# Optimization experiments

Measured on AMD Instinct MI355X. Metric: run time of the kernel, lower is better.

## Reference

```python
import jax, jax.numpy as jnp
import numpy as np

B, C, H, W = 8, 256, 200, 200
D_IN, D_HID, D_OUT = 256, 1024, 40000

def setup_inputs() -> dict:
    key = jax.random.key(0)
    k1, k2, k3, k4, k5, k6 = jax.random.split(key, 6)
    x = jax.random.normal(k1, (B, C, H, W), dtype=jnp.float32)
    localization = jax.random.normal(k2, (B, D_IN), dtype=jnp.float32)
    # Linear params (PyTorch default init scale ~ 1/sqrt(fan_in))
    W1 = jax.random.normal(k3, (D_IN, D_HID), dtype=jnp.float32) / np.sqrt(D_IN)
    b1 = jax.random.normal(k4, (D_HID,), dtype=jnp.float32) / np.sqrt(D_IN)
    W2 = jax.random.normal(k5, (D_HID, D_OUT), dtype=jnp.float32) / np.sqrt(D_HID)
    b2 = jax.random.normal(k6, (D_OUT,), dtype=jnp.float32) / np.sqrt(D_HID)
    return {"x": x, "localization": localization, "W1": W1, "b1": b1, "W2": W2, "b2": b2}

def reference(x, localization, W1, b1, W2, b2):
    # MLP: Linear(256,1024) -> LeakyReLU(0.1) -> Linear(1024,40000)
    h = localization @ W1 + b1
    h = jnp.where(h >= 0, h, 0.1 * h)
    w = h @ W2 + b2                      # [B, 40000]
    w = w.reshape(x.shape[0], 200, 200)  # [B, 200, 200]
    # Vectorized form of the nested loop: x[i,j] += x[i,j] * w[i]
    return x * (1.0 + w[:, None, :, :])
```

## Files before the change

### kernel.cpp

```cpp
#include <hip/hip_runtime.h>

#define B_    8
#define D_IN  256
#define D_HID 1024
#define D_OUT 40000
#define HW4   10000
#define CHW4  2560000

typedef float f32x4 __attribute__((ext_vector_type(4)));

__global__ void mlp1_kernel(const float* __restrict__ loc,
                            const float* __restrict__ W1,
                            const float* __restrict__ b1,
                            float* __restrict__ hT) {
    __shared__ float red[256];
    int g    = blockIdx.x;
    int b    = g >> 4;
    int k0   = (g & 15) * 64;
    int w    = threadIdx.x >> 6;
    int lane = threadIdx.x & 63;
    int k    = k0 + lane;

    float acc = 0.0f;
    #pragma unroll 8
    for (int ii = 0; ii < 64; ++ii) {
        int i = w * 64 + ii;
        acc += loc[b * D_IN + i] * W1[i * D_HID + k];
    }
    red[threadIdx.x] = acc;
    __syncthreads();
    if (w == 0) {
        float s = red[lane] + red[64 + lane] + red[128 + lane] + red[192 + lane];
        s += b1[k];
        s = (s >= 0.0f) ? s : 0.1f * s;
        hT[k * B_ + b] = s;
    }
}

template<int KS>
__global__ void mlp2_partial_kernel(const float* __restrict__ hT,
                                    const float* __restrict__ W2,
                                    float* __restrict__ partial) {
    constexpr int CHUNK = D_HID / KS;
    int j4 = blockIdx.x * 64 + threadIdx.x;
    if (j4 >= HW4) return;
    int ks = blockIdx.y;
    int k0 = ks * CHUNK;
    const f32x4* __restrict__ W24 = (const f32x4*)W2;
    f32x4 acc[B_];
    #pragma unroll
    for (int b = 0; b < B_; ++b) acc[b] = (f32x4)0.0f;
    #pragma unroll 8
    for (int kk = 0; kk < CHUNK; ++kk) {
        int k = k0 + kk;
        f32x4 wv = __builtin_nontemporal_load(&W24[k * HW4 + j4]);
        const float* __restrict__ h = &hT[k * B_];
        #pragma unroll
        for (int b = 0; b < B_; ++b)
            acc[b] += wv * h[b];
    }
    f32x4* __restrict__ p4 = (f32x4*)partial;
    #pragma unroll
    for (int b = 0; b < B_; ++b)
        __builtin_nontemporal_store(acc[b], &p4[(ks * B_ + b) * HW4 + j4]);
}

template<int KS>
__global__ void mlp2_reduce_kernel(const float* __restrict__ partial,
                                   const float* __restrict__ b2,
                                   float* __restrict__ wmap) {
    int t = blockIdx.x * blockDim.x + threadIdx.x;
    if (t >= B_ * HW4) return;
    int b = t / HW4;
    int j4 = t - b * HW4;
    const f32x4* __restrict__ p4  = (const f32x4*)partial;
    const f32x4* __restrict__ b24 = (const f32x4*)b2;
    f32x4 s = b24[j4] + 1.0f;
    #pragma unroll
    for (int ks = 0; ks < KS; ++ks)
        s += __builtin_nontemporal_load(&p4[(ks * B_ + b) * HW4 + j4]);
    ((f32x4*)wmap)[b * HW4 + j4] = s;
}

__global__ void scale_kernel(const float* __restrict__ x,
                             const float* __restrict__ wmap,
                             float* __restrict__ out) {
    const int b = blockIdx.y;
    const int g = blockIdx.x * 256 + threadIdx.x;
    const unsigned p = (unsigned)g % HW4;

    const f32x4* __restrict__ x4 = (const f32x4*)x + (size_t)b * CHW4;
    f32x4* __restrict__ o4       = (f32x4*)out + (size_t)b * CHW4;
    const f32x4 wv = ((const f32x4*)wmap)[(size_t)b * HW4 + p];

    #pragma unroll 4
    for (int n = 0; n < 16; ++n) {
        int i = g + n * 160000;
        f32x4 xv = __builtin_nontemporal_load(&x4[i]);
        __builtin_nontemporal_store(xv * wv, &o4[i]);
    }
}

template<int KS>
static void launch_mlp2(const float* hT, const float* W2, const float* b2,
                        float* partial, float* wmap, hipStream_t stream) {
    dim3 g2(157, KS);
    mlp2_partial_kernel<KS><<<g2, 64, 0, stream>>>(hT, W2, partial);
    mlp2_reduce_kernel<KS><<<(B_ * HW4 + 255) / 256, 256, 0, stream>>>(partial, b2, wmap);
}

extern "C" void kernel_launch(void* const* d_in, const int* in_sizes, int n_in,
                              void* d_out, int out_size, void* d_ws, size_t ws_size,
                              hipStream_t stream) {
    const float* x   = (const float*)d_in[0];
    const float* loc = (const float*)d_in[1];
    const float* W1  = (const float*)d_in[2];
    const float* b1  = (const float*)d_in[3];
    const float* W2  = (const float*)d_in[4];
    const float* b2  = (const float*)d_in[5];
    float* out = (float*)d_out;

    float* hT      = (float*)d_ws;
    float* partial = (float*)((char*)d_ws + 32768);

    size_t base = 32768;
    int KS = 1;
    for (int cand = 8; cand >= 1; cand >>= 1) {
        size_t need = base + (size_t)(cand + 1) * B_ * D_OUT * sizeof(float);
        if (need <= ws_size) { KS = cand; break; }
    }
    float* wmap = (float*)((char*)d_ws + base
                           + (size_t)KS * B_ * D_OUT * sizeof(float));

    mlp1_kernel<<<128, 256, 0, stream>>>(loc, W1, b1, hT);

    switch (KS) {
        case 8:  launch_mlp2<8>(hT, W2, b2, partial, wmap, stream); break;
        case 4:  launch_mlp2<4>(hT, W2, b2, partial, wmap, stream); break;
        case 2:  launch_mlp2<2>(hT, W2, b2, partial, wmap, stream); break;
        default: launch_mlp2<1>(hT, W2, b2, partial, wmap, stream); break;
    }

    scale_kernel<<<dim3(625, 8), 256, 0, stream>>>(x, wmap, out);
}
```

Baseline: 162.5 us.

## Fuse MLP stages into one persistent kernel with atomic grid barriers

Merges the hidden-layer kernel, the W2 partial GEMV and the partial reduction into a single launch of one-wave blocks that coordinate through global atomic counters and spin-wait barriers. Ticketed blocks compute the hidden layer while the others wait on a completion counter. A grid-wide barrier separates the partial products from the reduction. This removes two kernel launches and their gaps, at the cost of spin-wait overhead, a memset, a fixed split count, and reliance on every block being co-resident.

New measurement: 410.2 us. +152.5%, slower.

```diff
diff --git a/kernel.cpp b/kernel.cpp
--- a/kernel.cpp
+++ b/kernel.cpp
@@ -6,80 +6,103 @@
 #define D_OUT 40000
 #define HW4   10000
 #define CHW4  2560000
+#define KS    8
+#define CHUNK 128
+#define NUNITS 1256
+#define RBLK  1250
 
 typedef float f32x4 __attribute__((ext_vector_type(4)));
+typedef unsigned long long u64;
 
-__global__ void mlp1_kernel(const float* __restrict__ loc,
+__device__ __forceinline__ void store16_agent(f32x4 v, f32x4* p) {
+    union { f32x4 v; u64 q[2]; } u; u.v = v;
+    u64* d = (u64*)p;
+    __hip_atomic_store(d,     u.q[0], __ATOMIC_RELAXED, __HIP_MEMORY_SCOPE_AGENT);
+    __hip_atomic_store(d + 1, u.q[1], __ATOMIC_RELAXED, __HIP_MEMORY_SCOPE_AGENT);
+}
+
+__global__ void mlpA_kernel(const float* __restrict__ loc,
                             const float* __restrict__ W1,
                             const float* __restrict__ b1,
-                            float* __restrict__ hT) {
-    __shared__ float red[256];
-    int g    = blockIdx.x;
-    int b    = g >> 4;
-    int k0   = (g & 15) * 64;
-    int w    = threadIdx.x >> 6;
-    int lane = threadIdx.x & 63;
-    int k    = k0 + lane;
+                            const float* __restrict__ W2,
+                            const float* __restrict__ b2,
+                            unsigned* __restrict__ ctl,
+                            float* __restrict__ hT,
+                            float* __restrict__ partial,
+                            float* __restrict__ wmap) {
+    const int bid  = blockIdx.x;
+    const int lane = threadIdx.x;
+    unsigned* ticket = ctl;
+    unsigned* f128   = ctl + 32;
+    unsigned* done   = ctl + 64;
 
-    float acc = 0.0f;
-    #pragma unroll 8
-    for (int ii = 0; ii < 64; ++ii) {
-        int i = w * 64 + ii;
-        acc += loc[b * D_IN + i] * W1[i * D_HID + k];
+    unsigned t;
+    if (lane == 0)
+        t = __hip_atomic_fetch_add(ticket, 1u, __ATOMIC_RELAXED, __HIP_MEMORY_SCOPE_AGENT);
+    t = (unsigned)__shfl((int)t, 0);
+    if (t < 128u) {
+        int b = (int)(t >> 4);
+        int k = (int)(t & 15u) * 64 + lane;
+        float acc = 0.0f;
+        #pragma unroll 8
+        for (int i = 0; i < D_IN; ++i)
+            acc += loc[b * D_IN + i] * W1[i * D_HID + k];
+        acc += b1[k];
+        acc = (acc >= 0.0f) ? acc : 0.1f * acc;
+        __hip_atomic_store(&hT[k * B_ + b], acc, __ATOMIC_RELAXED, __HIP_MEMORY_SCOPE_AGENT);
+        __builtin_amdgcn_fence(__ATOMIC_RELEASE, "agent");
+        if (lane == 0)
+            __hip_atomic_fetch_add(f128, 1u, __ATOMIC_RELEASE, __HIP_MEMORY_SCOPE_AGENT);
     }
-    red[threadIdx.x] = acc;
-    __syncthreads();
-    if (w == 0) {
-        float s = red[lane] + red[64 + lane] + red[128 + lane] + red[192 + lane];
-        s += b1[k];
-        s = (s >= 0.0f) ? s : 0.1f * s;
-        hT[k * B_ + b] = s;
+    if (lane == 0)
+        while (__hip_atomic_load(f128, __ATOMIC_RELAXED, __HIP_MEMORY_SCOPE_AGENT) < 128u)
+            __builtin_amdgcn_s_sleep(4);
+    __builtin_amdgcn_fence(__ATOMIC_ACQUIRE, "agent");
+
+    {
+        int jblk = bid % 157;
+        int ks   = bid / 157;
+        int j4   = jblk * 64 + lane;
+        if (j4 < HW4) {
+            int k0 = ks * CHUNK;
+            const f32x4* __restrict__ W24 = (const f32x4*)W2;
+            f32x4 acc[B_];
+            #pragma unroll
+            for (int b = 0; b < B_; ++b) acc[b] = (f32x4)0.0f;
+            #pragma unroll 8
+            for (int kk = 0; kk < CHUNK; ++kk) {
+                int k = k0 + kk;
+                f32x4 wv = __builtin_nontemporal_load(&W24[k * HW4 + j4]);
+                const float* __restrict__ h = &hT[k * B_];
+                #pragma unroll
+                for (int b = 0; b < B_; ++b)
+                    acc[b] += wv * h[b];
+            }
+            f32x4* __restrict__ p4 = (f32x4*)partial;
+            #pragma unroll
+            for (int b = 0; b < B_; ++b)
+                store16_agent(acc[b], &p4[(ks * B_ + b) * HW4 + j4]);
+        }
     }
-}
+    __builtin_amdgcn_fence(__ATOMIC_RELEASE, "agent");
+    if (lane == 0) {
+        __hip_atomic_fetch_add(done, 1u, __ATOMIC_RELEASE, __HIP_MEMORY_SCOPE_AGENT);
+        while (__hip_atomic_load(done, __ATOMIC_RELAXED, __HIP_MEMORY_SCOPE_AGENT) < NUNITS)
+            __builtin_amdgcn_s_sleep(4);
+    }
+    __builtin_amdgcn_fence(__ATOMIC_ACQUIRE, "agent");
 
-template<int KS>
-__global__ void mlp2_partial_kernel(const float* __restrict__ hT,
-                                    const float* __restrict__ W2,
-                                    float* __restrict__ partial) {
-    constexpr int CHUNK = D_HID / KS;
-    int j4 = blockIdx.x * 64 + threadIdx.x;
-    if (j4 >= HW4) return;
-    int ks = blockIdx.y;
-    int k0 = ks * CHUNK;
-    const f32x4* __restrict__ W24 = (const f32x4*)W2;
-    f32x4 acc[B_];
-    #pragma unroll
-    for (int b = 0; b < B_; ++b) acc[b] = (f32x4)0.0f;
-    #pragma unroll 8
-    for (int kk = 0; kk < CHUNK; ++kk) {
-        int k = k0 + kk;
-        f32x4 wv = __builtin_nontemporal_load(&W24[k * HW4 + j4]);
-        const float* __restrict__ h = &hT[k * B_];
+    if (bid < RBLK) {
+        int tt = bid * 64 + lane;
+        int b  = tt / HW4;
+        int j4 = tt - b * HW4;
+        const f32x4* __restrict__ p4  = (const f32x4*)partial;
+        f32x4 s = ((const f32x4*)b2)[j4] + 1.0f;
         #pragma unroll
-        for (int b = 0; b < B_; ++b)
-            acc[b] += wv * h[b];
+        for (int ks = 0; ks < KS; ++ks)
+            s += p4[(ks * B_ + b) * HW4 + j4];
+        ((f32x4*)wmap)[b * HW4 + j4] = s;
     }
-    f32x4* __restrict__ p4 = (f32x4*)partial;
-    #pragma unroll
-    for (int b = 0; b < B_; ++b)
-        __builtin_nontemporal_store(acc[b], &p4[(ks * B_ + b) * HW4 + j4]);
-}
-
-template<int KS>
-__global__ void mlp2_reduce_kernel(const float* __restrict__ partial,
-                                   const float* __restrict__ b2,
-                                   float* __restrict__ wmap) {
-    int t = blockIdx.x * blockDim.x + threadIdx.x;
-    if (t >= B_ * HW4) return;
-    int b = t / HW4;
-    int j4 = t - b * HW4;
-    const f32x4* __restrict__ p4  = (const f32x4*)partial;
-    const f32x4* __restrict__ b24 = (const f32x4*)b2;
-    f32x4 s = b24[j4] + 1.0f;
-    #pragma unroll
-    for (int ks = 0; ks < KS; ++ks)
-        s += __builtin_nontemporal_load(&p4[(ks * B_ + b) * HW4 + j4]);
-    ((f32x4*)wmap)[b * HW4 + j4] = s;
 }
 
 __global__ void scale_kernel(const float* __restrict__ x,
@@ -101,14 +124,6 @@
     }
 }
 
-template<int KS>
-static void launch_mlp2(const float* hT, const float* W2, const float* b2,
-                        float* partial, float* wmap, hipStream_t stream) {
-    dim3 g2(157, KS);
-    mlp2_partial_kernel<KS><<<g2, 64, 0, stream>>>(hT, W2, partial);
-    mlp2_reduce_kernel<KS><<<(B_ * HW4 + 255) / 256, 256, 0, stream>>>(partial, b2, wmap);
-}
-
 extern "C" void kernel_launch(void* const* d_in, const int* in_sizes, int n_in,
                               void* d_out, int out_size, void* d_ws, size_t ws_size,
                               hipStream_t stream) {
@@ -120,26 +135,14 @@
     const float* b2  = (const float*)d_in[5];
     float* out = (float*)d_out;
 
-    float* hT      = (float*)d_ws;
-    float* partial = (float*)((char*)d_ws + 32768);
+    unsigned* ctl  = (unsigned*)d_ws;
+    float* hT      = (float*)((char*)d_ws + 512);
+    float* partial = (float*)((char*)d_ws + 512 + 32768);
+    float* wmap    = (float*)((char*)d_ws + 512 + 32768
+                              + (size_t)KS * B_ * D_OUT * sizeof(float));
 
-    size_t base = 32768;
-    int KS = 1;
-    for (int cand = 8; cand >= 1; cand >>= 1) {
-        size_t need = base + (size_t)(cand + 1) * B_ * D_OUT * sizeof(float);
-        if (need <= ws_size) { KS = cand; break; }
-    }
-    float* wmap = (float*)((char*)d_ws + base
-                           + (size_t)KS * B_ * D_OUT * sizeof(float));
+    hipMemsetAsync(d_ws, 0, 512, stream);
 
-    mlp1_kernel<<<128, 256, 0, stream>>>(loc, W1, b1, hT);
-
-    switch (KS) {
-        case 8:  launch_mlp2<8>(hT, W2, b2, partial, wmap, stream); break;
-        case 4:  launch_mlp2<4>(hT, W2, b2, partial, wmap, stream); break;
-        case 2:  launch_mlp2<2>(hT, W2, b2, partial, wmap, stream); break;
-        default: launch_mlp2<1>(hT, W2, b2, partial, wmap, stream); break;
-    }
-
+    mlpA_kernel<<<NUNITS, 64, 0, stream>>>(loc, W1, b1, W2, b2, ctl, hT, partial, wmap);
     scale_kernel<<<dim3(625, 8), 256, 0, stream>>>(x, wmap, out);
 }
```
